# Performance work log

Measured on AMD Instinct MI355X. Metric: run time of the kernel, lower is better.

Reference implementation:

```python
import jax, jax.numpy as jnp
import numpy as np

D_MODEL = 1024
NUM_EXPERTS = 16
TOP_K = 2
CAPACITY_FACTOR = 1.25
SINKHORN_ITERS = 3
AUX_LOSS_WEIGHT = 0.01


def setup_inputs() -> dict:
    key = jax.random.key(0)
    ks = jax.random.split(key, 6)
    d, e, h = D_MODEL, NUM_EXPERTS, 4 * D_MODEL
    sd = 1.0 / np.sqrt(d)
    sh = 1.0 / np.sqrt(h)
    return {
        "x": jax.random.normal(ks[0], (4, 2048, d), dtype=jnp.float32),
        "W_router": jax.random.uniform(ks[1], (d, e), jnp.float32, -sd, sd),
        "W1": jax.random.uniform(ks[2], (e, d, h), jnp.float32, -sd, sd),
        "b1": jax.random.uniform(ks[3], (e, h), jnp.float32, -sd, sd),
        "W2": jax.random.uniform(ks[4], (e, h, d), jnp.float32, -sh, sh),
        "b2": jax.random.uniform(ks[5], (e, d), jnp.float32, -sh, sh),
    }


def _moe_forward(x, W_router, W1, b1, W2, b2):
    B, S, D = x.shape
    E, K = NUM_EXPERTS, TOP_K
    N = B * S
    capacity = max(int(N * CAPACITY_FACTOR / E), K)  # static python int

    xf = x.reshape(N, D)
    router_logits = xf @ W_router                      # [N, E]
    probs = jax.nn.softmax(router_logits, axis=-1)
    # Sinkhorn balancing (as in source: row-normalize, col-normalize, rescale)
    for _ in range(SINKHORN_ITERS):
        probs = probs / probs.sum(axis=-1, keepdims=True)
        probs = probs / probs.sum(axis=0, keepdims=True)
        probs = probs * (N / E)

    weights, indices = jax.lax.top_k(probs, K)         # [N, K]
    weights = weights / weights.sum(axis=-1, keepdims=True)

    # --- dispatch: sequential slot allocation in (t, k) order ---
    flat_e = indices.reshape(-1)                       # [N*K]
    onehot = (flat_e[:, None] == jnp.arange(E)[None, :]).astype(jnp.int32)  # [N*K, E]
    # position of each dispatch within its expert = count of earlier same-expert entries
    pos = (jnp.cumsum(onehot, axis=0) * onehot).sum(-1) - 1                  # [N*K]
    mask = pos < capacity                              # dispatch_mask flattened
    total_counts = onehot.sum(0)                       # [E]
    token_counts = jnp.minimum(total_counts, capacity)

    safe_pos = jnp.where(mask, pos, 0)
    flat_idx = jnp.where(mask, flat_e * capacity + safe_pos, E * capacity)
    x_rep = jnp.repeat(xf, K, axis=0)                  # [N*K, D], (t,k) order
    buf = jnp.zeros((E * capacity + 1, D), dtype=x.dtype)
    buf = buf.at[flat_idx].set(x_rep)
    expert_input = buf[: E * capacity].reshape(E, capacity, D)

    # --- per-expert MLP (exact GELU, as torch.nn.GELU default) ---
    h = jnp.einsum('ecd,edf->ecf', expert_input, W1) + b1[:, None, :]
    h = jax.nn.gelu(h, approximate=False)
    expert_output = jnp.einsum('ecf,efd->ecd', h, W2) + b2[:, None, :]  # [E, cap, D]

    # --- weighted gather-combine ---
    gathered = expert_output[flat_e, safe_pos]         # [N*K, D]
    w = (weights.reshape(-1) * mask.astype(weights.dtype))[:, None]
    y = (gathered * w).reshape(N, K, D).sum(axis=1).reshape(B, S, D)

    aux_loss = AUX_LOSS_WEIGHT * E * (
        probs.mean(axis=0) * (token_counts.astype(probs.dtype) / N)
    ).sum()
    return y, aux_loss


def reference(x, W_router, W1, b1, W2, b2):
    return _moe_forward(x, W_router, W1, b1, W2, b2)
```

## Files before the change

kernel.cpp:

```cpp
#include <hip/hip_runtime.h>
#include <hip/hip_bf16.h>
#include <math.h>

#define NTOK 8192
#define DM   1024
#define NE   16
#define HD   4096
#define CAP  640
#define NCHUNK 64

typedef float f32x4 __attribute__((ext_vector_type(4)));
typedef _Float16 f16x8 __attribute__((ext_vector_type(8)));
typedef _Float16 f16x4 __attribute__((ext_vector_type(4)));

__device__ __forceinline__ void gload16(const void* g, void* l) {
  __builtin_amdgcn_global_load_lds(
      (const __attribute__((address_space(1))) unsigned int*)g,
      (__attribute__((address_space(3))) unsigned int*)l, 16, 0, 0);
}

__device__ __forceinline__ float gelu_fast(float v) {
  float v2 = v * v;
  float z2n = v * fmaf(-0.07135481627f, v2, -1.595769122f);
  float e = __expf(z2n);
  return v / (1.0f + e);
}

__global__ __launch_bounds__(256) void k_router(const float* __restrict__ x,
                                                const float* __restrict__ Wr,
                                                float* __restrict__ probs,
                                                float* __restrict__ pout) {
  int wave = threadIdx.x >> 6, lane = threadIdx.x & 63;
  int tok = blockIdx.x * 4 + wave;
  const float* xr = x + (size_t)tok * DM;
  float acc[NE];
#pragma unroll
  for (int e = 0; e < NE; ++e) acc[e] = 0.f;
  for (int d = lane; d < DM; d += 64) {
    float xv = xr[d];
    const float* w = Wr + (size_t)d * NE;
#pragma unroll
    for (int e = 0; e < NE; ++e) acc[e] = fmaf(xv, w[e], acc[e]);
  }
#pragma unroll
  for (int off = 32; off >= 1; off >>= 1) {
#pragma unroll
    for (int e = 0; e < NE; ++e) acc[e] += __shfl_xor(acc[e], off, 64);
  }
  float m = acc[0];
#pragma unroll
  for (int e = 1; e < NE; ++e) m = fmaxf(m, acc[e]);
  float s = 0.f;
#pragma unroll
  for (int e = 0; e < NE; ++e) { acc[e] = expf(acc[e] - m); s += acc[e]; }
  float inv = 1.0f / s;
#pragma unroll
  for (int e = 0; e < NE; ++e) acc[e] *= inv;
  if (lane < NE) probs[(size_t)tok * NE + lane] = acc[lane];
  __shared__ float wsum[4][NE];
  if (lane == 0) {
#pragma unroll
    for (int e = 0; e < NE; ++e) wsum[wave][e] = acc[e];
  }
  __syncthreads();
  if (threadIdx.x < NE)
    pout[blockIdx.x * NE + threadIdx.x] =
        wsum[0][threadIdx.x] + wsum[1][threadIdx.x] + wsum[2][threadIdx.x] + wsum[3][threadIdx.x];
}

__global__ __launch_bounds__(256) void k_sink(float* __restrict__ probs,
                                              const float* __restrict__ pin,
                                              float* __restrict__ pout) {
  __shared__ float csinv[NE];
  int tid = threadIdx.x;
  if (tid < NE) {
    float s = 0.f;
#pragma unroll
    for (int b = 0; b < 32; ++b) s += pin[b * NE + tid];
    csinv[tid] = 512.0f / s;
  }
  __syncthreads();
  int tok = blockIdx.x * 256 + tid;
  float* row = probs + (size_t)tok * NE;
  float p[NE]; float rs = 0.f;
#pragma unroll
  for (int e = 0; e < NE; ++e) { p[e] = row[e] * csinv[e]; rs += p[e]; }
  float rinv = 1.0f / rs;
#pragma unroll
  for (int e = 0; e < NE; ++e) { p[e] *= rinv; row[e] = p[e]; }
#pragma unroll
  for (int off = 32; off >= 1; off >>= 1) {
#pragma unroll
    for (int e = 0; e < NE; ++e) p[e] += __shfl_xor(p[e], off, 64);
  }
  __shared__ float wsum[4][NE];
  int lane = tid & 63, wave = tid >> 6;
  if (lane == 0) {
#pragma unroll
    for (int e = 0; e < NE; ++e) wsum[wave][e] = p[e];
  }
  __syncthreads();
  if (tid < NE)
    pout[blockIdx.x * NE + tid] =
        wsum[0][tid] + wsum[1][tid] + wsum[2][tid] + wsum[3][tid];
}

__global__ __launch_bounds__(256) void k_sink3(const float* __restrict__ probs,
                                               const float* __restrict__ pin,
                                               int* __restrict__ eidx,
                                               float* __restrict__ ew) {
  __shared__ float csinv[NE];
  int tid = threadIdx.x;
  if (tid < NE) {
    float s = 0.f;
#pragma unroll
    for (int b = 0; b < 32; ++b) s += pin[b * NE + tid];
    csinv[tid] = 512.0f / s;
  }
  __syncthreads();
  int tok = blockIdx.x * 256 + tid;
  const float* row = probs + (size_t)tok * NE;
  float v0 = -1e30f, v1 = -1e30f; int e0 = 0, e1 = 0;
#pragma unroll
  for (int e = 0; e < NE; ++e) {
    float v = row[e] * csinv[e];
    if (v > v0) { v1 = v0; e1 = e0; v0 = v; e0 = e; }
    else if (v > v1) { v1 = v; e1 = e; }
  }
  float s = v0 + v1;
  eidx[tok * 2] = e0; eidx[tok * 2 + 1] = e1;
  ew[tok * 2] = v0 / s; ew[tok * 2 + 1] = v1 / s;
}

__global__ __launch_bounds__(256) void k_hist(const int* __restrict__ eidx,
                                              int* __restrict__ cnt) {
  __shared__ int h[NE];
  int tid = threadIdx.x, c = blockIdx.x;
  if (tid < NE) h[tid] = 0;
  __syncthreads();
  atomicAdd(&h[eidx[c * 256 + tid]], 1);
  __syncthreads();
  if (tid < NE) cnt[c * NE + tid] = h[tid];
}

__global__ __launch_bounds__(64) void k_prefix(const int* __restrict__ cnt,
                                               int* __restrict__ base,
                                               int* __restrict__ counts,
                                               float* __restrict__ aux) {
  __shared__ int tot[NE];
  int e = threadIdx.x;
  if (e < NE) {
    int run = 0;
    for (int c = 0; c < NCHUNK; ++c) {
      base[c * NE + e] = run;
      run += cnt[c * NE + e];
    }
    counts[e] = run;
    tot[e] = min(run, CAP);
  }
  __syncthreads();
  if (e == 0) {
    int s = 0;
#pragma unroll
    for (int i = 0; i < NE; ++i) s += tot[i];
    *aux = 0.01f * (float)s / (float)NTOK;
  }
}

__global__ __launch_bounds__(256) void k_assign(const int* __restrict__ eidx,
                                                const int* __restrict__ base,
                                                int* __restrict__ slot_tok,
                                                int* __restrict__ tok2slot) {
  __shared__ int wcnt[4][NE];
  __shared__ int cbase[NE];
  int tid = threadIdx.x, c = blockIdx.x, lane = tid & 63, wave = tid >> 6;
  int i = c * 256 + tid;
  int myE = eidx[i];
  if (tid < NE) cbase[tid] = base[c * NE + tid];
  int mypre = 0;
#pragma unroll
  for (int e = 0; e < NE; ++e) {
    unsigned long long m = __ballot(myE == e);
    if (myE == e) mypre = __popcll(m & ((1ull << lane) - 1ull));
    if (lane == 0) wcnt[wave][e] = __popcll(m);
  }
  __syncthreads();
  int pre = 0;
  for (int w = 0; w < wave; ++w) pre += wcnt[w][myE];
  int pos = cbase[myE] + pre + mypre;
  if (pos < CAP) {
    slot_tok[myE * CAP + pos] = i >> 1;
    tok2slot[i] = myE * CAP + pos;
  } else {
    tok2slot[i] = -1;
  }
}

__global__ __launch_bounds__(256) void k_gather(const float* __restrict__ x,
                                                const int* __restrict__ slot_tok,
                                                _Float16* __restrict__ xg) {
  int row = blockIdx.x;
  int tok = slot_tok[row];
  int t = threadIdx.x;
  f16x4 h;
  if (tok >= 0) {
    float4 v = *(const float4*)(x + (size_t)tok * DM + t * 4);
    h[0] = (_Float16)v.x; h[1] = (_Float16)v.y; h[2] = (_Float16)v.z; h[3] = (_Float16)v.w;
  } else {
    h[0] = (_Float16)0.f; h[1] = (_Float16)0.f; h[2] = (_Float16)0.f; h[3] = (_Float16)0.f;
  }
  *(f16x4*)(xg + (size_t)row * DM + t * 4) = h;
}


__device__ __forceinline__ void stage_tileA128(const _Float16* gbase, int ld, int k0,
                                               _Float16* lds, int w, int lane) {
#pragma unroll
  for (int i = 0; i < 4; ++i) {
    int ci = (w * 4 + i) * 64 + lane;
    int row = ci >> 3, c = ci & 7;
    int cs = c ^ (row & 7);
    gload16(gbase + (size_t)row * ld + k0 + cs * 8, lds + (w * 4 + i) * 512);
  }
}

__device__ __forceinline__ void loadB8(const float* gb, int ld, int k0, int tid, float4* L) {
  int nq = tid & 31, kc = tid >> 5;
  const float* p = gb + (size_t)(k0 + kc * 8) * ld + nq * 4;
#pragma unroll
  for (int j = 0; j < 8; ++j) L[j] = *(const float4*)(p + (size_t)j * ld);
}

__device__ __forceinline__ void writeB(_Float16* Bs, int tid, const float4* L) {
  int nq = tid & 31, kc = tid >> 5;
#pragma unroll
  for (int i = 0; i < 4; ++i) {
    int n = nq * 4 + i;
    int pos = kc ^ ((n ^ (n >> 2)) & 7);
    f16x8 v;
#pragma unroll
    for (int j = 0; j < 8; ++j) {
      float f = (i == 0) ? L[j].x : (i == 1) ? L[j].y : (i == 2) ? L[j].z : L[j].w;
      v[j] = (_Float16)f;
    }
    *(f16x8*)(Bs + n * 64 + pos * 8) = v;
  }
}

#define MFMA_PHASE(Ac, Bs)                                                         \
  _Pragma("unroll")                                                                \
  for (int ks = 0; ks < 2; ++ks) {                                                 \
    f16x8 af[4], bf[4];                                                            \
    _Pragma("unroll")                                                              \
    for (int m = 0; m < 4; ++m) {                                                  \
      int row = wr * 64 + m * 16 + lr;                                             \
      int cs = (ks * 4 + kg) ^ (row & 7);                                          \
      af[m] = *(const f16x8*)((Ac) + row * 64 + cs * 8);                           \
    }                                                                              \
    _Pragma("unroll")                                                              \
    for (int n = 0; n < 4; ++n) {                                                  \
      int row = wc * 64 + n * 16 + lr;                                             \
      int cs = (ks * 4 + kg) ^ ((row ^ (row >> 2)) & 7);                           \
      bf[n] = *(const f16x8*)((Bs) + row * 64 + cs * 8);                           \
    }                                                                              \
    __builtin_amdgcn_s_setprio(1);                                                 \
    _Pragma("unroll")                                                              \
    for (int m = 0; m < 4; ++m)                                                    \
      _Pragma("unroll")                                                            \
      for (int n = 0; n < 4; ++n)                                                  \
        acc[m][n] = __builtin_amdgcn_mfma_f32_16x16x32_f16(af[m], bf[n], acc[m][n], 0, 0, 0); \
    __builtin_amdgcn_s_setprio(0);                                                 \
  }

#define ASYNC_K_LOOP(NT, AB, ALD, BB, BLD, KBASE)                                  \
  {                                                                                \
    stage_tileA128((AB), (ALD), (KBASE), As0, w, lane);                            \
    loadB8((BB), (BLD), (KBASE), tid, L);                                          \
    asm volatile("s_waitcnt vmcnt(0)" ::: "memory");                               \
    __builtin_amdgcn_s_barrier();                                                  \
    __builtin_amdgcn_sched_barrier(0);                                             \
    for (int t = 0; t < (NT); ++t) {                                               \
      const _Float16* Ac = (t & 1) ? As1 : As0;                                    \
      _Float16* An = (t & 1) ? As0 : As1;                                          \
      writeB(Bs, tid, L);                                                          \
      if (t + 1 < (NT)) {                                                          \
        stage_tileA128((AB), (ALD), (KBASE) + (t + 1) * 64, An, w, lane);          \
        loadB8((BB), (BLD), (KBASE) + (t + 1) * 64, tid, L);                       \
      }                                                                            \
      asm volatile("s_waitcnt lgkmcnt(0)" ::: "memory");                           \
      __builtin_amdgcn_s_barrier();                                                \
      __builtin_amdgcn_sched_barrier(0);                                           \
      MFMA_PHASE(Ac, Bs);                                                          \
      __builtin_amdgcn_sched_barrier(0);                                           \
      if (t + 1 < (NT)) { asm volatile("s_waitcnt vmcnt(8)" ::: "memory"); }       \
      else              { asm volatile("s_waitcnt vmcnt(0)" ::: "memory"); }       \
      __builtin_amdgcn_s_barrier();                                                \
      __builtin_amdgcn_sched_barrier(0);                                           \
    }                                                                              \
  }

__global__ __launch_bounds__(256) void k_gemm1(const _Float16* __restrict__ xg,
                                               const float* __restrict__ W1,
                                               const float* __restrict__ b1,
                                               _Float16* __restrict__ hbuf) {
  int bid = blockIdx.x;
  int logical = (bid & 7) * 320 + (bid >> 3);
  int my = logical % 5;
  int nx = (logical / 5) % 32;
  int e  = logical / 160;
  int m0 = my * 128, n0 = nx * 128;
  __shared__ _Float16 smem[3 * 128 * 64];
  _Float16* As0 = smem;
  _Float16* As1 = smem + 8192;
  _Float16* Bs  = smem + 16384;
  const _Float16* Ab = xg + ((size_t)e * CAP + m0) * DM;
  const float*    Bb = W1 + (size_t)e * DM * HD + n0;
  int tid = threadIdx.x, lane = tid & 63, w = tid >> 6;
  int wr = w >> 1, wc = w & 1;
  int lr = lane & 15, kg = lane >> 4;

  f32x4 acc[4][4];
#pragma unroll
  for (int m = 0; m < 4; ++m)
#pragma unroll
    for (int n = 0; n < 4; ++n) acc[m][n] = (f32x4){0.f, 0.f, 0.f, 0.f};

  float4 L[8];
  ASYNC_K_LOOP(16, Ab, DM, Bb, HD, 0);

  __syncthreads();
  _Float16* Cb = smem;
  int lq = lane >> 4;
#pragma unroll
  for (int n = 0; n < 4; ++n) {
    int col = wc * 64 + n * 16 + lr;
    float bias = b1[(size_t)e * HD + n0 + col];
#pragma unroll
    for (int m = 0; m < 4; ++m) {
#pragma unroll
      for (int r = 0; r < 4; ++r) {
        int row = wr * 64 + m * 16 + lq * 4 + r;
        float v = gelu_fast(acc[m][n][r] + bias);
        Cb[row * 128 + (col ^ (((row >> 2) & 3) << 4))] = (_Float16)v;
      }
    }
  }
  __syncthreads();
  int rr = tid >> 4;
  int c8 = (tid & 15) * 8;
#pragma unroll
  for (int p = 0; p < 8; ++p) {
    int row = p * 16 + rr;
    int colx = c8 ^ (((row >> 2) & 3) << 4);
    f16x8 v = *(const f16x8*)(Cb + row * 128 + colx);
    *(f16x8*)(hbuf + ((size_t)e * CAP + m0 + row) * HD + n0 + c8) = v;
  }
}

__global__ __launch_bounds__(256) void k_gemm2(const _Float16* __restrict__ hbuf,
                                               const float* __restrict__ W2,
                                               const float* __restrict__ b2,
                                               _Float16* __restrict__ P0,
                                               _Float16* __restrict__ P1) {
  int bid = blockIdx.x;
  int logical = (bid & 7) * 160 + (bid >> 3);
  int my = logical % 5;
  int nx = (logical / 5) % 8;
  int ks2 = (logical / 40) & 1;
  int e  = logical / 80;
  int m0 = my * 128, n0 = nx * 128, kbase = ks2 * 2048;
  __shared__ _Float16 smem[3 * 128 * 64];
  _Float16* As0 = smem;
  _Float16* As1 = smem + 8192;
  _Float16* Bs  = smem + 16384;
  const _Float16* Ab = hbuf + ((size_t)e * CAP + m0) * HD;
  const float*    Bb = W2 + (size_t)e * HD * DM + n0;
  int tid = threadIdx.x, lane = tid & 63, w = tid >> 6;
  int wr = w >> 1, wc = w & 1;
  int lr = lane & 15, kg = lane >> 4;

  f32x4 acc[4][4];
#pragma unroll
  for (int m = 0; m < 4; ++m)
#pragma unroll
    for (int n = 0; n < 4; ++n) acc[m][n] = (f32x4){0.f, 0.f, 0.f, 0.f};

  float4 L[8];
  ASYNC_K_LOOP(32, Ab, HD, Bb, DM, kbase);

  __syncthreads();
  _Float16* Cb = smem;
  _Float16* P = (ks2 == 0) ? P0 : P1;
  int lq = lane >> 4;
  float bias[4];
#pragma unroll
  for (int n = 0; n < 4; ++n)
    bias[n] = (ks2 == 0) ? b2[(size_t)e * DM + n0 + wc * 64 + n * 16 + lr] : 0.f;
#pragma unroll
  for (int m = 0; m < 4; ++m) {
#pragma unroll
    for (int n = 0; n < 4; ++n) {
#pragma unroll
      for (int r = 0; r < 4; ++r) {
        int row = wr * 64 + m * 16 + lq * 4 + r;
        int col = wc * 64 + n * 16 + lr;
        Cb[row * 128 + (col ^ (((row >> 2) & 3) << 4))] = (_Float16)(acc[m][n][r] + bias[n]);
      }
    }
  }
  __syncthreads();
  int rr = tid >> 4;
  int c8 = (tid & 15) * 8;
#pragma unroll
  for (int p = 0; p < 8; ++p) {
    int row = p * 16 + rr;
    int colx = c8 ^ (((row >> 2) & 3) << 4);
    f16x8 v = *(const f16x8*)(Cb + row * 128 + colx);
    *(f16x8*)(P + ((size_t)e * CAP + m0 + row) * DM + n0 + c8) = v;
  }
}

__global__ __launch_bounds__(256) void k_combine(const _Float16* __restrict__ P0,
                                                 const _Float16* __restrict__ P1,
                                                 const int* __restrict__ tok2slot,
                                                 const float* __restrict__ ew,
                                                 float* __restrict__ y) {
  int t = blockIdx.x;
  int d = threadIdx.x * 4;
  int i0 = tok2slot[t * 2], i1 = tok2slot[t * 2 + 1];
  float w0 = ew[t * 2], w1 = ew[t * 2 + 1];
  float a0 = 0.f, a1 = 0.f, a2 = 0.f, a3 = 0.f;
  if (i0 >= 0) {
    f16x4 oa = *(const f16x4*)(P0 + (size_t)i0 * DM + d);
    f16x4 ob = *(const f16x4*)(P1 + (size_t)i0 * DM + d);
    a0 += w0 * ((float)oa[0] + (float)ob[0]); a1 += w0 * ((float)oa[1] + (float)ob[1]);
    a2 += w0 * ((float)oa[2] + (float)ob[2]); a3 += w0 * ((float)oa[3] + (float)ob[3]);
  }
  if (i1 >= 0) {
    f16x4 oa = *(const f16x4*)(P0 + (size_t)i1 * DM + d);
    f16x4 ob = *(const f16x4*)(P1 + (size_t)i1 * DM + d);
    a0 += w1 * ((float)oa[0] + (float)ob[0]); a1 += w1 * ((float)oa[1] + (float)ob[1]);
    a2 += w1 * ((float)oa[2] + (float)ob[2]); a3 += w1 * ((float)oa[3] + (float)ob[3]);
  }
  float4 out = make_float4(a0, a1, a2, a3);
  *(float4*)(y + (size_t)t * DM + d) = out;
}

extern "C" void kernel_launch(void* const* d_in, const int* in_sizes, int n_in,
                              void* d_out, int out_size, void* d_ws, size_t ws_size,
                              hipStream_t stream) {
  const float* x  = (const float*)d_in[0];
  const float* Wr = (const float*)d_in[1];
  const float* W1 = (const float*)d_in[2];
  const float* b1 = (const float*)d_in[3];
  const float* W2 = (const float*)d_in[4];
  const float* b2 = (const float*)d_in[5];
  float* y = (float*)d_out;
  float* aux = y + (size_t)out_size - 1;

  char* ws = (char*)d_ws;
  float* probs    = (float*)ws; ws += (size_t)NTOK * NE * 4;
  float* C0       = (float*)ws; ws += 32 * NE * 4;
  float* C1       = (float*)ws; ws += 32 * NE * 4;
  int*   eidx     = (int*)ws;   ws += NTOK * 2 * 4;
  float* ew       = (float*)ws; ws += NTOK * 2 * 4;
  int*   slot_tok = (int*)ws;   ws += NE * CAP * 4;
  int*   tok2slot = (int*)ws;   ws += NTOK * 2 * 4;
  int*   counts   = (int*)ws;   ws += 256;
  int*   cnt      = (int*)ws;   ws += NCHUNK * NE * 4;
  int*   cbase    = (int*)ws;   ws += NCHUNK * NE * 4;
  _Float16* xg    = (_Float16*)ws; ws += (size_t)NE * CAP * DM * 2;
  _Float16* hbuf  = (_Float16*)ws; ws += (size_t)NE * CAP * HD * 2;
  _Float16* P1b   = (_Float16*)ws; ws += (size_t)NE * CAP * DM * 2;
  _Float16* P0b   = xg;

  hipMemsetAsync(slot_tok, 0xFF, (size_t)NE * CAP * 4, stream);

  k_router<<<NTOK / 4, 256, 0, stream>>>(x, Wr, probs, C0);
  k_sink<<<32, 256, 0, stream>>>(probs, C0, C1);
  k_sink<<<32, 256, 0, stream>>>(probs, C1, C0);
  k_sink3<<<32, 256, 0, stream>>>(probs, C0, eidx, ew);
  k_hist<<<NCHUNK, 256, 0, stream>>>(eidx, cnt);
  k_prefix<<<1, 64, 0, stream>>>(cnt, cbase, counts, aux);
  k_assign<<<NCHUNK, 256, 0, stream>>>(eidx, cbase, slot_tok, tok2slot);
  k_gather<<<NE * CAP, 256, 0, stream>>>(x, slot_tok, xg);

  k_gemm1<<<2560, 256, 0, stream>>>(xg, W1, b1, hbuf);
  k_gemm2<<<1280, 256, 0, stream>>>(hbuf, W2, b2, P0b, P1b);

  k_combine<<<NTOK, 256, 0, stream>>>(P0b, P1b, tok2slot, ew, y);
}
```

Before: 384.4 us.

## Double-buffer B tile in LDS and prefetch two stages ahead in GEMM loops

Adds a second LDS buffer for the W tile and restructures the K loop so the fp32-to-fp16 conversion and store of the next B tile, plus the global load for the tile two steps ahead, are issued before the MFMA phase of the current tile. This removes one barrier per iteration and is meant to overlap B conversion and global latency with compute. LDS per block rises from 48KB to 64KB of dynamic shared memory, which may lower the number of blocks resident per CU.

```diff
diff --git a/kernel.cpp b/kernel.cpp
--- a/kernel.cpp
+++ b/kernel.cpp
@@ -247,7 +247,7 @@
   }
 }
 
-#define MFMA_PHASE(Ac, Bs)                                                         \
+#define MFMA_PHASE(Ac, Bc)                                                         \
   _Pragma("unroll")                                                                \
   for (int ks = 0; ks < 2; ++ks) {                                                 \
     f16x8 af[4], bf[4];                                                            \
@@ -261,7 +261,7 @@
     for (int n = 0; n < 4; ++n) {                                                  \
       int row = wc * 64 + n * 16 + lr;                                             \
       int cs = (ks * 4 + kg) ^ ((row ^ (row >> 2)) & 7);                           \
-      bf[n] = *(const f16x8*)((Bs) + row * 64 + cs * 8);                           \
+      bf[n] = *(const f16x8*)((Bc) + row * 64 + cs * 8);                           \
     }                                                                              \
     __builtin_amdgcn_s_setprio(1);                                                 \
     _Pragma("unroll")                                                              \
@@ -274,26 +274,38 @@
 
 #define ASYNC_K_LOOP(NT, AB, ALD, BB, BLD, KBASE)                                  \
   {                                                                                \
+                              \
+    loadB8((BB), (BLD), (KBASE), tid, L);                                          \
     stage_tileA128((AB), (ALD), (KBASE), As0, w, lane);                            \
-    loadB8((BB), (BLD), (KBASE), tid, L);                                          \
-    asm volatile("s_waitcnt vmcnt(0)" ::: "memory");                               \
+    __builtin_amdgcn_sched_barrier(0);                                             \
+    writeB(Bs0, tid, L);                                                           \
+    __builtin_amdgcn_sched_barrier(0);                                             \
+    if ((NT) > 1) loadB8((BB), (BLD), (KBASE) + 64, tid, L);                       \
+    __builtin_amdgcn_sched_barrier(0);                                             \
+    asm volatile("s_waitcnt lgkmcnt(0)" ::: "memory");                             \
+    if ((NT) > 1) { asm volatile("s_waitcnt vmcnt(8)" ::: "memory"); }             \
+    else          { asm volatile("s_waitcnt vmcnt(0)" ::: "memory"); }             \
     __builtin_amdgcn_s_barrier();                                                  \
     __builtin_amdgcn_sched_barrier(0);                                             \
     for (int t = 0; t < (NT); ++t) {                                               \
       const _Float16* Ac = (t & 1) ? As1 : As0;                                    \
+      const _Float16* Bc = (t & 1) ? Bs1 : Bs0;                                    \
       _Float16* An = (t & 1) ? As0 : As1;                                          \
-      writeB(Bs, tid, L);                                                          \
-      if (t + 1 < (NT)) {                                                          \
-        stage_tileA128((AB), (ALD), (KBASE) + (t + 1) * 64, An, w, lane);          \
-        loadB8((BB), (BLD), (KBASE) + (t + 1) * 64, tid, L);                       \
+      _Float16* Bn = (t & 1) ? Bs0 : Bs1;                                          \
+      bool pf1 = (t + 1) < (NT);                                                   \
+      bool pf2 = (t + 2) < (NT);                                                   \
+      if (pf1) stage_tileA128((AB), (ALD), (KBASE) + (t + 1) * 64, An, w, lane);   \
+      __builtin_amdgcn_sched_barrier(0);                                           \
+      if (pf1) writeB(Bn, tid, L);                 \
+      __builtin_amdgcn_sched_barrier(0);                                           \
+      if (pf2) loadB8((BB), (BLD), (KBASE) + (t + 2) * 64, tid, L);                \
+      __builtin_amdgcn_sched_barrier(0);                                           \
+      MFMA_PHASE(Ac, Bc);                                                          \
+      asm volatile("s_waitcnt lgkmcnt(0)" ::: "memory");                           \
+      if (pf1) {                                                                   \
+        if (pf2) { asm volatile("s_waitcnt vmcnt(8)" ::: "memory"); }              \
+        else     { asm volatile("s_waitcnt vmcnt(0)" ::: "memory"); }              \
       }                                                                            \
-      asm volatile("s_waitcnt lgkmcnt(0)" ::: "memory");                           \
-      __builtin_amdgcn_s_barrier();                                                \
-      __builtin_amdgcn_sched_barrier(0);                                           \
-      MFMA_PHASE(Ac, Bs);                                                          \
-      __builtin_amdgcn_sched_barrier(0);                                           \
-      if (t + 1 < (NT)) { asm volatile("s_waitcnt vmcnt(8)" ::: "memory"); }       \
-      else              { asm volatile("s_waitcnt vmcnt(0)" ::: "memory"); }       \
       __builtin_amdgcn_s_barrier();                                                \
       __builtin_amdgcn_sched_barrier(0);                                           \
     }                                                                              \
@@ -303,16 +315,17 @@
                                                const float* __restrict__ W1,
                                                const float* __restrict__ b1,
                                                _Float16* __restrict__ hbuf) {
+  extern __shared__ _Float16 smem[];
+  _Float16* As0 = smem;
+  _Float16* As1 = smem + 8192;
+  _Float16* Bs0 = smem + 16384;
+  _Float16* Bs1 = smem + 24576;
   int bid = blockIdx.x;
   int logical = (bid & 7) * 320 + (bid >> 3);
   int my = logical % 5;
   int nx = (logical / 5) % 32;
   int e  = logical / 160;
   int m0 = my * 128, n0 = nx * 128;
-  __shared__ _Float16 smem[3 * 128 * 64];
-  _Float16* As0 = smem;
-  _Float16* As1 = smem + 8192;
-  _Float16* Bs  = smem + 16384;
   const _Float16* Ab = xg + ((size_t)e * CAP + m0) * DM;
   const float*    Bb = W1 + (size_t)e * DM * HD + n0;
   int tid = threadIdx.x, lane = tid & 63, w = tid >> 6;
@@ -362,6 +375,11 @@
                                                const float* __restrict__ b2,
                                                _Float16* __restrict__ P0,
                                                _Float16* __restrict__ P1) {
+  extern __shared__ _Float16 smem[];
+  _Float16* As0 = smem;
+  _Float16* As1 = smem + 8192;
+  _Float16* Bs0 = smem + 16384;
+  _Float16* Bs1 = smem + 24576;
   int bid = blockIdx.x;
   int logical = (bid & 7) * 160 + (bid >> 3);
   int my = logical % 5;
@@ -369,10 +387,6 @@
   int ks2 = (logical / 40) & 1;
   int e  = logical / 80;
   int m0 = my * 128, n0 = nx * 128, kbase = ks2 * 2048;
-  __shared__ _Float16 smem[3 * 128 * 64];
-  _Float16* As0 = smem;
-  _Float16* As1 = smem + 8192;
-  _Float16* Bs  = smem + 16384;
   const _Float16* Ab = hbuf + ((size_t)e * CAP + m0) * HD;
   const float*    Bb = W2 + (size_t)e * HD * DM + n0;
   int tid = threadIdx.x, lane = tid & 63, w = tid >> 6;
@@ -474,6 +488,9 @@
   _Float16* P1b   = (_Float16*)ws; ws += (size_t)NE * CAP * DM * 2;
   _Float16* P0b   = xg;
 
+  hipFuncSetAttribute((const void*)k_gemm1, hipFuncAttributeMaxDynamicSharedMemorySize, 65536);
+  hipFuncSetAttribute((const void*)k_gemm2, hipFuncAttributeMaxDynamicSharedMemorySize, 65536);
+
   hipMemsetAsync(slot_tok, 0xFF, (size_t)NE * CAP * 4, stream);
 
   k_router<<<NTOK / 4, 256, 0, stream>>>(x, Wr, probs, C0);
@@ -485,8 +502,8 @@
   k_assign<<<NCHUNK, 256, 0, stream>>>(eidx, cbase, slot_tok, tok2slot);
   k_gather<<<NE * CAP, 256, 0, stream>>>(x, slot_tok, xg);
 
-  k_gemm1<<<2560, 256, 0, stream>>>(xg, W1, b1, hbuf);
-  k_gemm2<<<1280, 256, 0, stream>>>(hbuf, W2, b2, P0b, P1b);
+  k_gemm1<<<2560, 256, 65536, stream>>>(xg, W1, b1, hbuf);
+  k_gemm2<<<1280, 256, 65536, stream>>>(hbuf, W2, b2, P0b, P1b);
 
   k_combine<<<NTOK, 256, 0, stream>>>(P0b, P1b, tok2slot, ew, y);
 }
```

New measurement: 398.4 us. +3.6%, slower.

## Widen expert GEMM tiles to 128x256 with 512 threads and 4-way split-K

Applied to the files above, without the earlier changes.

Both expert GEMMs now use 512-thread blocks that compute 128x256 output tiles, with 8 waves arranged 2x4, so each block reads more of the f32 weight matrix per staged A tile. The shared-memory layout grows to 64 KB of dynamic LDS. The second GEMM switches from 2-way to 4-way split-K, writing four partial buffers that the combine kernel sums. The aim is to cut A-tile reloads and raise per-block reuse of the weights, at the cost of higher register and LDS pressure, lower occupancy and more partial-sum traffic in combine.

```diff
diff --git a/kernel.cpp b/kernel.cpp
--- a/kernel.cpp
+++ b/kernel.cpp
@@ -213,26 +213,26 @@
 }
 
 
-__device__ __forceinline__ void stage_tileA128(const _Float16* gbase, int ld, int k0,
+__device__ __forceinline__ void stage_tileA512(const _Float16* gbase, int ld, int k0,
                                                _Float16* lds, int w, int lane) {
 #pragma unroll
-  for (int i = 0; i < 4; ++i) {
-    int ci = (w * 4 + i) * 64 + lane;
+  for (int i = 0; i < 2; ++i) {
+    int ci = (w * 2 + i) * 64 + lane;
     int row = ci >> 3, c = ci & 7;
     int cs = c ^ (row & 7);
-    gload16(gbase + (size_t)row * ld + k0 + cs * 8, lds + (w * 4 + i) * 512);
+    gload16(gbase + (size_t)row * ld + k0 + cs * 8, lds + (w * 2 + i) * 512);
   }
 }
 
 __device__ __forceinline__ void loadB8(const float* gb, int ld, int k0, int tid, float4* L) {
-  int nq = tid & 31, kc = tid >> 5;
+  int nq = tid & 63, kc = tid >> 6;
   const float* p = gb + (size_t)(k0 + kc * 8) * ld + nq * 4;
 #pragma unroll
   for (int j = 0; j < 8; ++j) L[j] = *(const float4*)(p + (size_t)j * ld);
 }
 
 __device__ __forceinline__ void writeB(_Float16* Bs, int tid, const float4* L) {
-  int nq = tid & 31, kc = tid >> 5;
+  int nq = tid & 63, kc = tid >> 6;
 #pragma unroll
   for (int i = 0; i < 4; ++i) {
     int n = nq * 4 + i;
@@ -247,7 +247,7 @@
   }
 }
 
-#define MFMA_PHASE(Ac, Bs)                                                         \
+#define MFMA_PHASE(Ac, Bsb)                                                        \
   _Pragma("unroll")                                                                \
   for (int ks = 0; ks < 2; ++ks) {                                                 \
     f16x8 af[4], bf[4];                                                            \
@@ -261,7 +261,7 @@
     for (int n = 0; n < 4; ++n) {                                                  \
       int row = wc * 64 + n * 16 + lr;                                             \
       int cs = (ks * 4 + kg) ^ ((row ^ (row >> 2)) & 7);                           \
-      bf[n] = *(const f16x8*)((Bs) + row * 64 + cs * 8);                           \
+      bf[n] = *(const f16x8*)((Bsb) + row * 64 + cs * 8);                          \
     }                                                                              \
     __builtin_amdgcn_s_setprio(1);                                                 \
     _Pragma("unroll")                                                              \
@@ -274,7 +274,7 @@
 
 #define ASYNC_K_LOOP(NT, AB, ALD, BB, BLD, KBASE)                                  \
   {                                                                                \
-    stage_tileA128((AB), (ALD), (KBASE), As0, w, lane);                            \
+    stage_tileA512((AB), (ALD), (KBASE), As0, w, lane);                            \
     loadB8((BB), (BLD), (KBASE), tid, L);                                          \
     asm volatile("s_waitcnt vmcnt(0)" ::: "memory");                               \
     __builtin_amdgcn_s_barrier();                                                  \
@@ -283,9 +283,12 @@
       const _Float16* Ac = (t & 1) ? As1 : As0;                                    \
       _Float16* An = (t & 1) ? As0 : As1;                                          \
       writeB(Bs, tid, L);                                                          \
+      __builtin_amdgcn_sched_barrier(0);                                           \
       if (t + 1 < (NT)) {                                                          \
-        stage_tileA128((AB), (ALD), (KBASE) + (t + 1) * 64, An, w, lane);          \
+        stage_tileA512((AB), (ALD), (KBASE) + (t + 1) * 64, An, w, lane);          \
+        __builtin_amdgcn_sched_barrier(0);                                         \
         loadB8((BB), (BLD), (KBASE) + (t + 1) * 64, tid, L);                       \
+        __builtin_amdgcn_sched_barrier(0);                                         \
       }                                                                            \
       asm volatile("s_waitcnt lgkmcnt(0)" ::: "memory");                           \
       __builtin_amdgcn_s_barrier();                                                \
@@ -299,24 +302,24 @@
     }                                                                              \
   }
 
-__global__ __launch_bounds__(256) void k_gemm1(const _Float16* __restrict__ xg,
+__global__ __launch_bounds__(512) void k_gemm1(const _Float16* __restrict__ xg,
                                                const float* __restrict__ W1,
                                                const float* __restrict__ b1,
                                                _Float16* __restrict__ hbuf) {
-  int bid = blockIdx.x;
-  int logical = (bid & 7) * 320 + (bid >> 3);
-  int my = logical % 5;
-  int nx = (logical / 5) % 32;
-  int e  = logical / 160;
-  int m0 = my * 128, n0 = nx * 128;
-  __shared__ _Float16 smem[3 * 128 * 64];
+  extern __shared__ _Float16 smem[];
   _Float16* As0 = smem;
   _Float16* As1 = smem + 8192;
   _Float16* Bs  = smem + 16384;
+  int bid = blockIdx.x;
+  int logical = (bid & 7) * 160 + (bid >> 3);
+  int my = logical % 5;
+  int nx = (logical / 5) % 16;
+  int e  = logical / 80;
+  int m0 = my * 128, n0 = nx * 256;
   const _Float16* Ab = xg + ((size_t)e * CAP + m0) * DM;
   const float*    Bb = W1 + (size_t)e * DM * HD + n0;
   int tid = threadIdx.x, lane = tid & 63, w = tid >> 6;
-  int wr = w >> 1, wc = w & 1;
+  int wr = w >> 2, wc = w & 3;
   int lr = lane & 15, kg = lane >> 4;
 
   f32x4 acc[4][4];
@@ -341,42 +344,44 @@
       for (int r = 0; r < 4; ++r) {
         int row = wr * 64 + m * 16 + lq * 4 + r;
         float v = gelu_fast(acc[m][n][r] + bias);
-        Cb[row * 128 + (col ^ (((row >> 2) & 3) << 4))] = (_Float16)v;
+        Cb[row * 256 + (col ^ (((row >> 2) & 3) << 4))] = (_Float16)v;
       }
     }
   }
   __syncthreads();
-  int rr = tid >> 4;
-  int c8 = (tid & 15) * 8;
+  int rr = tid >> 5;
+  int c8 = (tid & 31) * 8;
 #pragma unroll
   for (int p = 0; p < 8; ++p) {
     int row = p * 16 + rr;
     int colx = c8 ^ (((row >> 2) & 3) << 4);
-    f16x8 v = *(const f16x8*)(Cb + row * 128 + colx);
+    f16x8 v = *(const f16x8*)(Cb + row * 256 + colx);
     *(f16x8*)(hbuf + ((size_t)e * CAP + m0 + row) * HD + n0 + c8) = v;
   }
 }
 
-__global__ __launch_bounds__(256) void k_gemm2(const _Float16* __restrict__ hbuf,
+__global__ __launch_bounds__(512) void k_gemm2(const _Float16* __restrict__ hbuf,
                                                const float* __restrict__ W2,
                                                const float* __restrict__ b2,
                                                _Float16* __restrict__ P0,
-                                               _Float16* __restrict__ P1) {
+                                               _Float16* __restrict__ P1,
+                                               _Float16* __restrict__ P2,
+                                               _Float16* __restrict__ P3) {
+  extern __shared__ _Float16 smem[];
+  _Float16* As0 = smem;
+  _Float16* As1 = smem + 8192;
+  _Float16* Bs  = smem + 16384;
   int bid = blockIdx.x;
   int logical = (bid & 7) * 160 + (bid >> 3);
   int my = logical % 5;
-  int nx = (logical / 5) % 8;
-  int ks2 = (logical / 40) & 1;
+  int nx = (logical / 5) & 3;
+  int ks4 = (logical / 20) & 3;
   int e  = logical / 80;
-  int m0 = my * 128, n0 = nx * 128, kbase = ks2 * 2048;
-  __shared__ _Float16 smem[3 * 128 * 64];
-  _Float16* As0 = smem;
-  _Float16* As1 = smem + 8192;
-  _Float16* Bs  = smem + 16384;
+  int m0 = my * 128, n0 = nx * 256, kbase = ks4 * 1024;
   const _Float16* Ab = hbuf + ((size_t)e * CAP + m0) * HD;
   const float*    Bb = W2 + (size_t)e * HD * DM + n0;
   int tid = threadIdx.x, lane = tid & 63, w = tid >> 6;
-  int wr = w >> 1, wc = w & 1;
+  int wr = w >> 2, wc = w & 3;
   int lr = lane & 15, kg = lane >> 4;
 
   f32x4 acc[4][4];
@@ -386,16 +391,16 @@
     for (int n = 0; n < 4; ++n) acc[m][n] = (f32x4){0.f, 0.f, 0.f, 0.f};
 
   float4 L[8];
-  ASYNC_K_LOOP(32, Ab, HD, Bb, DM, kbase);
+  ASYNC_K_LOOP(16, Ab, HD, Bb, DM, kbase);
 
   __syncthreads();
   _Float16* Cb = smem;
-  _Float16* P = (ks2 == 0) ? P0 : P1;
+  _Float16* P = (ks4 == 0) ? P0 : (ks4 == 1) ? P1 : (ks4 == 2) ? P2 : P3;
   int lq = lane >> 4;
   float bias[4];
 #pragma unroll
   for (int n = 0; n < 4; ++n)
-    bias[n] = (ks2 == 0) ? b2[(size_t)e * DM + n0 + wc * 64 + n * 16 + lr] : 0.f;
+    bias[n] = (ks4 == 0) ? b2[(size_t)e * DM + n0 + wc * 64 + n * 16 + lr] : 0.f;
 #pragma unroll
   for (int m = 0; m < 4; ++m) {
 #pragma unroll
@@ -404,45 +409,47 @@
       for (int r = 0; r < 4; ++r) {
         int row = wr * 64 + m * 16 + lq * 4 + r;
         int col = wc * 64 + n * 16 + lr;
-        Cb[row * 128 + (col ^ (((row >> 2) & 3) << 4))] = (_Float16)(acc[m][n][r] + bias[n]);
+        Cb[row * 256 + (col ^ (((row >> 2) & 3) << 4))] = (_Float16)(acc[m][n][r] + bias[n]);
       }
     }
   }
   __syncthreads();
-  int rr = tid >> 4;
-  int c8 = (tid & 15) * 8;
+  int rr = tid >> 5;
+  int c8 = (tid & 31) * 8;
 #pragma unroll
   for (int p = 0; p < 8; ++p) {
     int row = p * 16 + rr;
     int colx = c8 ^ (((row >> 2) & 3) << 4);
-    f16x8 v = *(const f16x8*)(Cb + row * 128 + colx);
+    f16x8 v = *(const f16x8*)(Cb + row * 256 + colx);
     *(f16x8*)(P + ((size_t)e * CAP + m0 + row) * DM + n0 + c8) = v;
   }
 }
 
 __global__ __launch_bounds__(256) void k_combine(const _Float16* __restrict__ P0,
                                                  const _Float16* __restrict__ P1,
+                                                 const _Float16* __restrict__ P2,
+                                                 const _Float16* __restrict__ P3,
                                                  const int* __restrict__ tok2slot,
                                                  const float* __restrict__ ew,
                                                  float* __restrict__ y) {
   int t = blockIdx.x;
   int d = threadIdx.x * 4;
-  int i0 = tok2slot[t * 2], i1 = tok2slot[t * 2 + 1];
-  float w0 = ew[t * 2], w1 = ew[t * 2 + 1];
-  float a0 = 0.f, a1 = 0.f, a2 = 0.f, a3 = 0.f;
-  if (i0 >= 0) {
-    f16x4 oa = *(const f16x4*)(P0 + (size_t)i0 * DM + d);
-    f16x4 ob = *(const f16x4*)(P1 + (size_t)i0 * DM + d);
-    a0 += w0 * ((float)oa[0] + (float)ob[0]); a1 += w0 * ((float)oa[1] + (float)ob[1]);
-    a2 += w0 * ((float)oa[2] + (float)ob[2]); a3 += w0 * ((float)oa[3] + (float)ob[3]);
-  }
-  if (i1 >= 0) {
-    f16x4 oa = *(const f16x4*)(P0 + (size_t)i1 * DM + d);
-    f16x4 ob = *(const f16x4*)(P1 + (size_t)i1 * DM + d);
-    a0 += w1 * ((float)oa[0] + (float)ob[0]); a1 += w1 * ((float)oa[1] + (float)ob[1]);
-    a2 += w1 * ((float)oa[2] + (float)ob[2]); a3 += w1 * ((float)oa[3] + (float)ob[3]);
-  }
-  float4 out = make_float4(a0, a1, a2, a3);
+  float a[4] = {0.f, 0.f, 0.f, 0.f};
+#pragma unroll
+  for (int k = 0; k < 2; ++k) {
+    int idx = tok2slot[t * 2 + k];
+    if (idx >= 0) {
+      float wk = ew[t * 2 + k];
+      f16x4 o0 = *(const f16x4*)(P0 + (size_t)idx * DM + d);
+      f16x4 o1 = *(const f16x4*)(P1 + (size_t)idx * DM + d);
+      f16x4 o2 = *(const f16x4*)(P2 + (size_t)idx * DM + d);
+      f16x4 o3 = *(const f16x4*)(P3 + (size_t)idx * DM + d);
+#pragma unroll
+      for (int j = 0; j < 4; ++j)
+        a[j] += wk * ((float)o0[j] + (float)o1[j] + (float)o2[j] + (float)o3[j]);
+    }
+  }
+  float4 out = make_float4(a[0], a[1], a[2], a[3]);
   *(float4*)(y + (size_t)t * DM + d) = out;
 }
 
@@ -472,7 +479,12 @@
   _Float16* xg    = (_Float16*)ws; ws += (size_t)NE * CAP * DM * 2;
   _Float16* hbuf  = (_Float16*)ws; ws += (size_t)NE * CAP * HD * 2;
   _Float16* P1b   = (_Float16*)ws; ws += (size_t)NE * CAP * DM * 2;
+  _Float16* P2b   = (_Float16*)ws; ws += (size_t)NE * CAP * DM * 2;
+  _Float16* P3b   = (_Float16*)ws; ws += (size_t)NE * CAP * DM * 2;
   _Float16* P0b   = xg;
+
+  hipFuncSetAttribute((const void*)k_gemm1, hipFuncAttributeMaxDynamicSharedMemorySize, 65536);
+  hipFuncSetAttribute((const void*)k_gemm2, hipFuncAttributeMaxDynamicSharedMemorySize, 65536);
 
   hipMemsetAsync(slot_tok, 0xFF, (size_t)NE * CAP * 4, stream);
 
@@ -485,8 +497,8 @@
   k_assign<<<NCHUNK, 256, 0, stream>>>(eidx, cbase, slot_tok, tok2slot);
   k_gather<<<NE * CAP, 256, 0, stream>>>(x, slot_tok, xg);
 
-  k_gemm1<<<2560, 256, 0, stream>>>(xg, W1, b1, hbuf);
-  k_gemm2<<<1280, 256, 0, stream>>>(hbuf, W2, b2, P0b, P1b);
-
-  k_combine<<<NTOK, 256, 0, stream>>>(P0b, P1b, tok2slot, ew, y);
-}
+  k_gemm1<<<1280, 512, 65536, stream>>>(xg, W1, b1, hbuf);
+  k_gemm2<<<1280, 512, 65536, stream>>>(hbuf, W2, b2, P0b, P1b, P2b, P3b);
+
+  k_combine<<<NTOK, 256, 0, stream>>>(P0b, P1b, P2b, P3b, tok2slot, ew, y);
+}
```

After: 425.8 us. 1.11x slower.
